# Performance work log

Measured on AMD Instinct MI355X. Metric: run time of the kernel, lower is better.

## Reference

```python
import jax, jax.numpy as jnp
import numpy as np

BITWIDTH = 7
M, K, N = 32768, 1024, 1024  # tokens, in_features, out_features


def _clip8(x):
    return jnp.clip(x, -127, 127).astype(jnp.int8)


def _range_bits(x):
    # RangeEstimate: ceil(log2(max|x|)) as int, 0 if all-zero
    r = jnp.max(jnp.abs(x).astype(jnp.float32))
    bits = jnp.ceil(jnp.log2(jnp.maximum(r, 1.0)))
    return jnp.where(r == 0, 0, bits).astype(jnp.int32)


def _round_shift(x, shift):
    # RoundShift (stochastic-style bit-shift rounding); shift is a traced int32 >= 1
    p = jnp.left_shift(jnp.int32(1), shift)
    rt = jnp.floor_divide(x, p)
    prob = x - rt * p
    dec = jnp.floor_divide(prob, jnp.left_shift(jnp.int32(1), shift - 1))
    return _clip8(rt + dec)


def setup_inputs() -> dict:
    key = jax.random.key(0)
    k1, k2 = jax.random.split(key)
    act_in = jax.random.randint(k1, (M, K), -127, 128, dtype=jnp.int32).astype(jnp.int8)
    weight = jax.random.randint(k2, (N, K), -127, 128, dtype=jnp.int32).astype(jnp.int8)
    exp_in = jnp.int32(0)
    weight_exp = jnp.int32(-11)  # ceil(log2(xavier bound)) - 7 for 1024x1024
    return {"act_in": act_in, "weight": weight, "exp_in": exp_in, "weight_exp": weight_exp}


def reference(act_in, weight, exp_in, weight_exp):
    # int8 GEMM with int32 accumulation: [M,K] @ [K,N]
    acc = jnp.matmul(act_in.astype(jnp.int32), weight.T.astype(jnp.int32))
    # act_calc: range-estimate + conditional bit-shift requantize to int8
    bits = _range_bits(acc)
    shift = bits - BITWIDTH
    pos = shift > 0
    sc = jnp.maximum(shift, 1)  # safe shift for the untaken branch
    act_out = jnp.where(pos, _round_shift(acc, sc), acc.astype(jnp.int8))
    exp_out = jnp.where(pos, exp_in + weight_exp + shift, exp_in + weight_exp)
    return act_out, exp_out
```

## Files before the change

### kernel.cpp

```cpp
#include <hip/hip_runtime.h>
#include <stdint.h>


#define MM 32768
#define NN 1024
#define KK 1024
#define BM 256
#define BN 256
#define BK 64
#define NKT (KK / BK)

typedef __attribute__((ext_vector_type(4))) int i32x4;
typedef __attribute__((ext_vector_type(16))) int i32x16;

__device__ __forceinline__ int pack4(int a, int b, int c, int d) {
  return (int)((unsigned)(a & 0xff) | ((unsigned)(b & 0xff) << 8) |
               ((unsigned)(c & 0xff) << 16) | ((unsigned)(d & 0xff) << 24));
}

__global__ void k_init(unsigned* slot) {
  if (threadIdx.x == 0) *slot = 0u;
}

__global__ void k_pack(const int* __restrict__ src, int8_t* __restrict__ dst, int n) {
  long t = (long)blockIdx.x * blockDim.x + threadIdx.x;
  long stride = (long)gridDim.x * blockDim.x;
  for (long i = t * 16; i < (long)n; i += stride * 16) {
    const i32x4* s = (const i32x4*)(src + i);
    i32x4 a0 = s[0], a1 = s[1], a2 = s[2], a3 = s[3];
    i32x4 o;
    o[0] = pack4(a0[0], a0[1], a0[2], a0[3]);
    o[1] = pack4(a1[0], a1[1], a1[2], a1[3]);
    o[2] = pack4(a2[0], a2[1], a2[2], a2[3]);
    o[3] = pack4(a3[0], a3[1], a3[2], a3[3]);
    *(i32x4*)(dst + i) = o;
  }
}

__global__ __launch_bounds__(512, 2)
void k_gemm(const int8_t* __restrict__ A8, const int8_t* __restrict__ B8,
            int* __restrict__ out, unsigned* __restrict__ maxslot) {
  __shared__ int8_t As[2][BM * BK];
  __shared__ int8_t Bs[2][BN * BK];

  const int tid  = threadIdx.x;
  const int lane = tid & 63;
  const int w    = tid >> 6;
  const int wm   = w >> 2;
  const int wn   = w & 3;

  const int orig = blockIdx.x;
  const int wgid = ((orig & 7) << 6) + (orig >> 3);
  const int bn = wgid & 3;
  const int bm = wgid >> 2;
  const int m0 = bm * BM;
  const int n0 = bn * BN;

  i32x16 acc[4][2];
#pragma unroll
  for (int i = 0; i < 4; ++i)
#pragma unroll
    for (int j = 0; j < 2; ++j) acc[i][j] = 0;

  auto stage = [&](int buf, int kt) {
    const int k0 = kt * BK;
#pragma unroll
    for (int q = 0; q < 2; ++q) {
      const int p   = (w * 2 + q) * 1024 + lane * 16;
      const int row = p >> 6;
      const int col = (p & 63) ^ (((row >> 1) & 3) << 4);
      __builtin_amdgcn_global_load_lds(
          (const __attribute__((address_space(1))) void*)(A8 + (size_t)(m0 + row) * KK + k0 + col),
          (__attribute__((address_space(3))) void*)(&As[buf][(w * 2 + q) * 1024]),
          16, 0, 0);
      __builtin_amdgcn_global_load_lds(
          (const __attribute__((address_space(1))) void*)(B8 + (size_t)(n0 + row) * KK + k0 + col),
          (__attribute__((address_space(3))) void*)(&Bs[buf][(w * 2 + q) * 1024]),
          16, 0, 0);
    }
  };

  auto compute = [&](int buf) {
#pragma unroll
    for (int ks = 0; ks < 2; ++ks) {
      i32x4 af[4], bf[2];
#pragma unroll
      for (int ni = 0; ni < 2; ++ni) {
        const int row = wn * 64 + ni * 32 + (lane & 31);
        const int a = row * BK +
            ((ks * 32 + ((lane >> 5) << 4)) ^ (((row >> 1) & 3) << 4));
        bf[ni] = *(const i32x4*)(&Bs[buf][a]);
      }
#pragma unroll
      for (int mi = 0; mi < 4; ++mi) {
        const int row = wm * 128 + mi * 32 + (lane & 31);
        const int a = row * BK +
            ((ks * 32 + ((lane >> 5) << 4)) ^ (((row >> 1) & 3) << 4));
        af[mi] = *(const i32x4*)(&As[buf][a]);
      }
      __builtin_amdgcn_s_setprio(1);
#pragma unroll
      for (int mi = 0; mi < 4; ++mi)
#pragma unroll
        for (int ni = 0; ni < 2; ++ni)
          acc[mi][ni] = __builtin_amdgcn_mfma_i32_32x32x32_i8(
              af[mi], bf[ni], acc[mi][ni], 0, 0, 0);
      __builtin_amdgcn_s_setprio(0);
    }
  };

  stage(0, 0);
  __syncthreads();
  for (int kt = 0; kt < NKT; ++kt) {
    if (kt + 1 < NKT) stage((kt + 1) & 1, kt + 1);
    compute(kt & 1);
    __syncthreads();
  }

  int mx = 0;
#pragma unroll
  for (int mi = 0; mi < 4; ++mi)
#pragma unroll
    for (int ni = 0; ni < 2; ++ni)
#pragma unroll
      for (int rg = 0; rg < 16; ++rg) {
        int x = acc[mi][ni][rg];
        int a = x < 0 ? -x : x;
        mx = a > mx ? a : mx;
      }
#pragma unroll
  for (int off = 32; off >= 1; off >>= 1) {
    int o = __shfl_xor(mx, off);
    mx = o > mx ? o : mx;
  }
  if (lane == 0) atomicMax(maxslot, (unsigned)mx);

#pragma unroll
  for (int mi = 0; mi < 4; ++mi)
#pragma unroll
    for (int ni = 0; ni < 2; ++ni) {
      const int mbase = m0 + wm * 128 + mi * 32;
      const int ncol  = n0 + wn * 64 + ni * 32 + (lane & 31);
#pragma unroll
      for (int rg = 0; rg < 16; ++rg) {
        const int mrow = mbase + (rg & 3) + ((rg >> 2) << 3) + ((lane >> 5) << 2);
        out[(size_t)mrow * NN + ncol] = acc[mi][ni][rg];
      }
    }
}

__global__ __launch_bounds__(256, 2)
void k_gemm_fb(const int* __restrict__ A32, const int* __restrict__ B32,
               int* __restrict__ out, unsigned* __restrict__ maxslot) {
  __shared__ int8_t As[128 * 128];
  __shared__ int8_t Bs[128 * 128];
  const int tid = threadIdx.x, lane = tid & 63, w = tid >> 6;
  const int wr = w >> 1, wc = w & 1;
  const int bn = blockIdx.x & 7, bm = blockIdx.x >> 3;
  const int m0 = bm * 128, n0 = bn * 128;
  i32x16 acc[2][2];
#pragma unroll
  for (int i = 0; i < 2; ++i)
#pragma unroll
    for (int j = 0; j < 2; ++j) acc[i][j] = 0;
  for (int kt = 0; kt < 8; ++kt) {
    const int k0 = kt * 128;
    __syncthreads();
#pragma unroll
    for (int j = 0; j < 4; ++j) {
      const int fb = (j * 256 + tid) * 16;
      const int row = fb >> 7;
      const int swz = fb ^ ((row & 7) << 4);
      const int col = fb & 127;
      const int* sa = A32 + (size_t)(m0 + row) * KK + k0 + col;
      const int* sb = B32 + (size_t)(n0 + row) * KK + k0 + col;
      i32x4 av, bv;
#pragma unroll
      for (int t = 0; t < 4; ++t) {
        i32x4 ta = ((const i32x4*)sa)[t];
        i32x4 tb = ((const i32x4*)sb)[t];
        av[t] = pack4(ta[0], ta[1], ta[2], ta[3]);
        bv[t] = pack4(tb[0], tb[1], tb[2], tb[3]);
      }
      *(i32x4*)(As + swz) = av;
      *(i32x4*)(Bs + swz) = bv;
    }
    __syncthreads();
#pragma unroll
    for (int ks = 0; ks < 4; ++ks) {
      i32x4 af[2], bf[2];
#pragma unroll
      for (int mi = 0; mi < 2; ++mi) {
        const int row = wr * 64 + mi * 32 + (lane & 31);
        int a = row * 128 + ks * 32 + ((lane >> 5) << 4);
        a ^= (row & 7) << 4;
        af[mi] = *(const i32x4*)(As + a);
      }
#pragma unroll
      for (int ni = 0; ni < 2; ++ni) {
        const int row = wc * 64 + ni * 32 + (lane & 31);
        int a = row * 128 + ks * 32 + ((lane >> 5) << 4);
        a ^= (row & 7) << 4;
        bf[ni] = *(const i32x4*)(Bs + a);
      }
#pragma unroll
      for (int mi = 0; mi < 2; ++mi)
#pragma unroll
        for (int ni = 0; ni < 2; ++ni)
          acc[mi][ni] = __builtin_amdgcn_mfma_i32_32x32x32_i8(
              af[mi], bf[ni], acc[mi][ni], 0, 0, 0);
    }
  }
  int mx = 0;
#pragma unroll
  for (int mi = 0; mi < 2; ++mi)
#pragma unroll
    for (int ni = 0; ni < 2; ++ni)
#pragma unroll
      for (int rg = 0; rg < 16; ++rg) {
        int x = acc[mi][ni][rg];
        int a = x < 0 ? -x : x;
        mx = a > mx ? a : mx;
      }
#pragma unroll
  for (int off = 32; off >= 1; off >>= 1) {
    int o = __shfl_xor(mx, off);
    mx = o > mx ? o : mx;
  }
  if (lane == 0) atomicMax(maxslot, (unsigned)mx);
#pragma unroll
  for (int mi = 0; mi < 2; ++mi)
#pragma unroll
    for (int ni = 0; ni < 2; ++ni) {
      const int mbase = m0 + wr * 64 + mi * 32;
      const int ncol = n0 + wc * 64 + ni * 32 + (lane & 31);
#pragma unroll
      for (int rg = 0; rg < 16; ++rg) {
        const int mrow = mbase + (rg & 3) + ((rg >> 2) << 3) + ((lane >> 5) << 2);
        out[(size_t)mrow * NN + ncol] = acc[mi][ni][rg];
      }
    }
}

__global__ __launch_bounds__(256)
void k_requant(int* __restrict__ out, const unsigned* __restrict__ maxslot) {
  const unsigned r = *maxslot;
  const int bits  = (r <= 1u) ? 0 : (32 - __clz((int)(r - 1u)));
  const int shift = bits - 7;
  const size_t n = (size_t)MM * NN;
  size_t i = ((size_t)blockIdx.x * blockDim.x + threadIdx.x) * 4;
  const size_t stride = (size_t)gridDim.x * blockDim.x * 4;
  if (shift > 0) {
    for (; i < n; i += stride) {
      i32x4 v = *(i32x4*)(out + i);
#pragma unroll
      for (int j = 0; j < 4; ++j) {
        const int x = v[j];
        int t = (x >> shift) + ((x >> (shift - 1)) & 1);
        v[j] = t > 127 ? 127 : (t < -127 ? -127 : t);
      }
      *(i32x4*)(out + i) = v;
    }
  } else {
    for (; i < n; i += stride) {
      i32x4 v = *(i32x4*)(out + i);
#pragma unroll
      for (int j = 0; j < 4; ++j) v[j] = (int)(int8_t)v[j];
      *(i32x4*)(out + i) = v;
    }
  }
}

__global__ void k_final(int* __restrict__ out, const int* __restrict__ exp_in,
                        const int* __restrict__ wexp) {
  if (threadIdx.x == 0) {
    const unsigned r = *(const unsigned*)(out + (size_t)MM * NN);
    const int bits  = (r <= 1u) ? 0 : (32 - __clz((int)(r - 1u)));
    const int shift = bits - 7;
    out[(size_t)MM * NN] = *exp_in + *wexp + (shift > 0 ? shift : 0);
  }
}

extern "C" void kernel_launch(void* const* d_in, const int* in_sizes, int n_in,
                              void* d_out, int out_size, void* d_ws, size_t ws_size,
                              hipStream_t stream) {
  const int* act    = (const int*)d_in[0];
  const int* wgt    = (const int*)d_in[1];
  const int* exp_in = (const int*)d_in[2];
  const int* wexp   = (const int*)d_in[3];
  int* out          = (int*)d_out;
  unsigned* maxslot = (unsigned*)(out + (size_t)MM * NN);

  const size_t need = (size_t)(MM + NN) * KK + 256;

  k_init<<<1, 64, 0, stream>>>(maxslot);

  if (ws_size >= need) {
    int8_t* a8 = (int8_t*)d_ws;
    int8_t* w8 = a8 + (size_t)MM * KK;
    k_pack<<<2048, 256, 0, stream>>>(act, a8, MM * KK);
    k_pack<<<256, 256, 0, stream>>>(wgt, w8, NN * KK);
    const int grid = (MM / BM) * (NN / BN);
    k_gemm<<<grid, 512, 0, stream>>>(a8, w8, out, maxslot);
  } else {
    k_gemm_fb<<<(MM / 128) * (NN / 128), 256, 0, stream>>>(act, wgt, out, maxslot);
  }

  k_requant<<<4096, 256, 0, stream>>>(out, maxslot);
  k_final<<<1, 64, 0, stream>>>(out, exp_in, wexp);
}
```

Baseline: 173.8 us.

## Shrink GEMM tile to 256x128 and use triple-buffered LDS with partial waitcnt

Halves the N tile so each of the 8 warps computes a 64x64 sub-tile, which doubles the block count and cuts accumulator registers per thread. The LDS double buffer becomes a triple buffer with prefetch two k-steps ahead. __syncthreads is replaced by an explicit s_waitcnt vmcnt(3) plus s_barrier, so loads for the next stage can stay in flight during compute. Smaller tiles raise global traffic per MFMA, and the hand-counted vmcnt has to match the number of loads issued per stage (3 per stage here).

After: 195.9 us. +12.7%, slower.

```diff
diff --git a/kernel.cpp b/kernel.cpp
--- a/kernel.cpp
+++ b/kernel.cpp
@@ -6,12 +6,16 @@
 #define NN 1024
 #define KK 1024
 #define BM 256
-#define BN 256
+#define BN 128
 #define BK 64
 #define NKT (KK / BK)
+#define TSA (BM * BK)
+#define TSB (BN * BK)
 
 typedef __attribute__((ext_vector_type(4))) int i32x4;
 typedef __attribute__((ext_vector_type(16))) int i32x16;
+
+#define BARRIER() asm volatile("s_barrier" ::: "memory")
 
 __device__ __forceinline__ int pack4(int a, int b, int c, int d) {
   return (int)((unsigned)(a & 0xff) | ((unsigned)(b & 0xff) << 8) |
@@ -40,25 +44,25 @@
 __global__ __launch_bounds__(512, 2)
 void k_gemm(const int8_t* __restrict__ A8, const int8_t* __restrict__ B8,
             int* __restrict__ out, unsigned* __restrict__ maxslot) {
-  __shared__ int8_t As[2][BM * BK];
-  __shared__ int8_t Bs[2][BN * BK];
+  __shared__ int8_t As[3][TSA];
+  __shared__ int8_t Bs[3][TSB];
 
   const int tid  = threadIdx.x;
   const int lane = tid & 63;
   const int w    = tid >> 6;
-  const int wm   = w >> 2;
-  const int wn   = w & 3;
+  const int wm   = w >> 1;
+  const int wn   = w & 1;
 
   const int orig = blockIdx.x;
-  const int wgid = ((orig & 7) << 6) + (orig >> 3);
-  const int bn = wgid & 3;
-  const int bm = wgid >> 2;
+  const int wgid = ((orig & 7) << 7) + (orig >> 3);
+  const int bn = wgid & 7;
+  const int bm = wgid >> 3;
   const int m0 = bm * BM;
   const int n0 = bn * BN;
 
-  i32x16 acc[4][2];
-#pragma unroll
-  for (int i = 0; i < 4; ++i)
+  i32x16 acc[2][2];
+#pragma unroll
+  for (int i = 0; i < 2; ++i)
 #pragma unroll
     for (int j = 0; j < 2; ++j) acc[i][j] = 0;
 
@@ -73,9 +77,14 @@
           (const __attribute__((address_space(1))) void*)(A8 + (size_t)(m0 + row) * KK + k0 + col),
           (__attribute__((address_space(3))) void*)(&As[buf][(w * 2 + q) * 1024]),
           16, 0, 0);
+    }
+    {
+      const int p   = w * 1024 + lane * 16;
+      const int row = p >> 6;
+      const int col = (p & 63) ^ (((row >> 1) & 3) << 4);
       __builtin_amdgcn_global_load_lds(
           (const __attribute__((address_space(1))) void*)(B8 + (size_t)(n0 + row) * KK + k0 + col),
-          (__attribute__((address_space(3))) void*)(&Bs[buf][(w * 2 + q) * 1024]),
+          (__attribute__((address_space(3))) void*)(&Bs[buf][w * 1024]),
           16, 0, 0);
     }
   };
@@ -83,7 +92,7 @@
   auto compute = [&](int buf) {
 #pragma unroll
     for (int ks = 0; ks < 2; ++ks) {
-      i32x4 af[4], bf[2];
+      i32x4 af[2], bf[2];
 #pragma unroll
       for (int ni = 0; ni < 2; ++ni) {
         const int row = wn * 64 + ni * 32 + (lane & 31);
@@ -92,15 +101,15 @@
         bf[ni] = *(const i32x4*)(&Bs[buf][a]);
       }
 #pragma unroll
-      for (int mi = 0; mi < 4; ++mi) {
-        const int row = wm * 128 + mi * 32 + (lane & 31);
+      for (int mi = 0; mi < 2; ++mi) {
+        const int row = wm * 64 + mi * 32 + (lane & 31);
         const int a = row * BK +
             ((ks * 32 + ((lane >> 5) << 4)) ^ (((row >> 1) & 3) << 4));
         af[mi] = *(const i32x4*)(&As[buf][a]);
       }
       __builtin_amdgcn_s_setprio(1);
 #pragma unroll
-      for (int mi = 0; mi < 4; ++mi)
+      for (int mi = 0; mi < 2; ++mi)
 #pragma unroll
         for (int ni = 0; ni < 2; ++ni)
           acc[mi][ni] = __builtin_amdgcn_mfma_i32_32x32x32_i8(
@@ -110,16 +119,26 @@
   };
 
   stage(0, 0);
-  __syncthreads();
+  stage(1, 1);
+  asm volatile("s_waitcnt vmcnt(3)" ::: "memory");
+  BARRIER();
+
+  int b0 = 0, b1 = 1, b2 = 2;
   for (int kt = 0; kt < NKT; ++kt) {
-    if (kt + 1 < NKT) stage((kt + 1) & 1, kt + 1);
-    compute(kt & 1);
-    __syncthreads();
+    const bool more2 = (kt + 2 < NKT);
+    if (more2) stage(b2, kt + 2);
+    compute(b0);
+    if (kt + 1 < NKT) {
+      if (more2) { asm volatile("s_waitcnt vmcnt(3)" ::: "memory"); }
+      else       { asm volatile("s_waitcnt vmcnt(0)" ::: "memory"); }
+      BARRIER();
+    }
+    const int t = b0; b0 = b1; b1 = b2; b2 = t;
   }
 
   int mx = 0;
 #pragma unroll
-  for (int mi = 0; mi < 4; ++mi)
+  for (int mi = 0; mi < 2; ++mi)
 #pragma unroll
     for (int ni = 0; ni < 2; ++ni)
 #pragma unroll
@@ -136,10 +155,10 @@
   if (lane == 0) atomicMax(maxslot, (unsigned)mx);
 
 #pragma unroll
-  for (int mi = 0; mi < 4; ++mi)
+  for (int mi = 0; mi < 2; ++mi)
 #pragma unroll
     for (int ni = 0; ni < 2; ++ni) {
-      const int mbase = m0 + wm * 128 + mi * 32;
+      const int mbase = m0 + wm * 64 + mi * 32;
       const int ncol  = n0 + wn * 64 + ni * 32 + (lane & 31);
 #pragma unroll
       for (int rg = 0; rg < 16; ++rg) {
```

## Fuse int32-to-int8 activation packing into GEMM tile loads and merge small kernels

Applied to the files above, without the earlier changes.

Removes the separate activation pack pass. The GEMM now loads int32 activations directly, packs them to int8 in registers and stores them into the swizzled LDS tile. The max-slot reset moves into the weight pack kernel, and the exponent output is written by the requant kernel, which cuts two tiny launches. The trade-off is that A is now loaded synchronously at four times the bytes, reread by each N-block, instead of through async global-to-LDS loads. That could hurt GEMM pipelining. In the fallback path the exponent write can also race with other blocks reading maxslot.

Measured after the change: 176.8 us. No clear change (+1.7%).

```diff
diff --git a/kernel.cpp b/kernel.cpp
--- a/kernel.cpp
+++ b/kernel.cpp
@@ -18,11 +18,9 @@
                ((unsigned)(c & 0xff) << 16) | ((unsigned)(d & 0xff) << 24));
 }
 
-__global__ void k_init(unsigned* slot) {
-  if (threadIdx.x == 0) *slot = 0u;
-}
-
-__global__ void k_pack(const int* __restrict__ src, int8_t* __restrict__ dst, int n) {
+__global__ void k_packw(const int* __restrict__ src, int8_t* __restrict__ dst,
+                        unsigned* __restrict__ maxslot, int n) {
+  if (blockIdx.x == 0 && threadIdx.x == 0) *maxslot = 0u;
   long t = (long)blockIdx.x * blockDim.x + threadIdx.x;
   long stride = (long)gridDim.x * blockDim.x;
   for (long i = t * 16; i < (long)n; i += stride * 16) {
@@ -38,7 +36,7 @@
 }
 
 __global__ __launch_bounds__(512, 2)
-void k_gemm(const int8_t* __restrict__ A8, const int8_t* __restrict__ B8,
+void k_gemm(const int* __restrict__ A32, const int8_t* __restrict__ B8,
             int* __restrict__ out, unsigned* __restrict__ maxslot) {
   __shared__ int8_t As[2][BM * BK];
   __shared__ int8_t Bs[2][BN * BK];
@@ -70,13 +68,17 @@
       const int row = p >> 6;
       const int col = (p & 63) ^ (((row >> 1) & 3) << 4);
       __builtin_amdgcn_global_load_lds(
-          (const __attribute__((address_space(1))) void*)(A8 + (size_t)(m0 + row) * KK + k0 + col),
-          (__attribute__((address_space(3))) void*)(&As[buf][(w * 2 + q) * 1024]),
-          16, 0, 0);
-      __builtin_amdgcn_global_load_lds(
           (const __attribute__((address_space(1))) void*)(B8 + (size_t)(n0 + row) * KK + k0 + col),
           (__attribute__((address_space(3))) void*)(&Bs[buf][(w * 2 + q) * 1024]),
           16, 0, 0);
+      const int* sa = A32 + (size_t)(m0 + row) * KK + k0 + col;
+      i32x4 av;
+#pragma unroll
+      for (int t = 0; t < 4; ++t) {
+        i32x4 ta = ((const i32x4*)sa)[t];
+        av[t] = pack4(ta[0], ta[1], ta[2], ta[3]);
+      }
+      *(i32x4*)(&As[buf][p]) = av;
     }
   };
 
@@ -147,6 +149,42 @@
         out[(size_t)mrow * NN + ncol] = acc[mi][ni][rg];
       }
     }
+}
+
+__global__ __launch_bounds__(256)
+void k_requant(int* __restrict__ out, const unsigned* __restrict__ maxslot,
+               const int* __restrict__ exp_in, const int* __restrict__ wexp) {
+  const unsigned r = *maxslot;
+  const int bits  = (r <= 1u) ? 0 : (32 - __clz((int)(r - 1u)));
+  const int shift = bits - 7;
+  if (blockIdx.x == 0 && threadIdx.x == 0)
+    out[(size_t)MM * NN] = *exp_in + *wexp + (shift > 0 ? shift : 0);
+  const size_t n = (size_t)MM * NN;
+  size_t i = ((size_t)blockIdx.x * blockDim.x + threadIdx.x) * 4;
+  const size_t stride = (size_t)gridDim.x * blockDim.x * 4;
+  if (shift > 0) {
+    for (; i < n; i += stride) {
+      i32x4 v = *(i32x4*)(out + i);
+#pragma unroll
+      for (int j = 0; j < 4; ++j) {
+        const int x = v[j];
+        int t = (x >> shift) + ((x >> (shift - 1)) & 1);
+        v[j] = t > 127 ? 127 : (t < -127 ? -127 : t);
+      }
+      *(i32x4*)(out + i) = v;
+    }
+  } else {
+    for (; i < n; i += stride) {
+      i32x4 v = *(i32x4*)(out + i);
+#pragma unroll
+      for (int j = 0; j < 4; ++j) v[j] = (int)(int8_t)v[j];
+      *(i32x4*)(out + i) = v;
+    }
+  }
+}
+
+__global__ void k_init(unsigned* slot) {
+  if (threadIdx.x == 0) *slot = 0u;
 }
 
 __global__ __launch_bounds__(256, 2)
@@ -242,45 +280,6 @@
     }
 }
 
-__global__ __launch_bounds__(256)
-void k_requant(int* __restrict__ out, const unsigned* __restrict__ maxslot) {
-  const unsigned r = *maxslot;
-  const int bits  = (r <= 1u) ? 0 : (32 - __clz((int)(r - 1u)));
-  const int shift = bits - 7;
-  const size_t n = (size_t)MM * NN;
-  size_t i = ((size_t)blockIdx.x * blockDim.x + threadIdx.x) * 4;
-  const size_t stride = (size_t)gridDim.x * blockDim.x * 4;
-  if (shift > 0) {
-    for (; i < n; i += stride) {
-      i32x4 v = *(i32x4*)(out + i);
-#pragma unroll
-      for (int j = 0; j < 4; ++j) {
-        const int x = v[j];
-        int t = (x >> shift) + ((x >> (shift - 1)) & 1);
-        v[j] = t > 127 ? 127 : (t < -127 ? -127 : t);
-      }
-      *(i32x4*)(out + i) = v;
-    }
-  } else {
-    for (; i < n; i += stride) {
-      i32x4 v = *(i32x4*)(out + i);
-#pragma unroll
-      for (int j = 0; j < 4; ++j) v[j] = (int)(int8_t)v[j];
-      *(i32x4*)(out + i) = v;
-    }
-  }
-}
-
-__global__ void k_final(int* __restrict__ out, const int* __restrict__ exp_in,
-                        const int* __restrict__ wexp) {
-  if (threadIdx.x == 0) {
-    const unsigned r = *(const unsigned*)(out + (size_t)MM * NN);
-    const int bits  = (r <= 1u) ? 0 : (32 - __clz((int)(r - 1u)));
-    const int shift = bits - 7;
-    out[(size_t)MM * NN] = *exp_in + *wexp + (shift > 0 ? shift : 0);
-  }
-}
-
 extern "C" void kernel_launch(void* const* d_in, const int* in_sizes, int n_in,
                               void* d_out, int out_size, void* d_ws, size_t ws_size,
                               hipStream_t stream) {
@@ -289,23 +288,19 @@
   const int* exp_in = (const int*)d_in[2];
   const int* wexp   = (const int*)d_in[3];
   int* out          = (int*)d_out;
-  unsigned* maxslot = (unsigned*)(out + (size_t)MM * NN);
-
-  const size_t need = (size_t)(MM + NN) * KK + 256;
-
-  k_init<<<1, 64, 0, stream>>>(maxslot);
+
+  const size_t need = (size_t)NN * KK + 256;
 
   if (ws_size >= need) {
-    int8_t* a8 = (int8_t*)d_ws;
-    int8_t* w8 = a8 + (size_t)MM * KK;
-    k_pack<<<2048, 256, 0, stream>>>(act, a8, MM * KK);
-    k_pack<<<256, 256, 0, stream>>>(wgt, w8, NN * KK);
-    const int grid = (MM / BM) * (NN / BN);
-    k_gemm<<<grid, 512, 0, stream>>>(a8, w8, out, maxslot);
+    int8_t* w8 = (int8_t*)d_ws;
+    unsigned* maxslot = (unsigned*)(w8 + (size_t)NN * KK);
+    k_packw<<<256, 256, 0, stream>>>(wgt, w8, maxslot, NN * KK);
+    k_gemm<<<(MM / BM) * (NN / BN), 512, 0, stream>>>(act, w8, out, maxslot);
+    k_requant<<<4096, 256, 0, stream>>>(out, maxslot, exp_in, wexp);
   } else {
+    unsigned* maxslot = (unsigned*)(out + (size_t)MM * NN);
+    k_init<<<1, 64, 0, stream>>>(maxslot);
     k_gemm_fb<<<(MM / 128) * (NN / 128), 256, 0, stream>>>(act, wgt, out, maxslot);
-  }
-
-  k_requant<<<4096, 256, 0, stream>>>(out, maxslot);
-  k_final<<<1, 64, 0, stream>>>(out, exp_in, wexp);
-}
+    k_requant<<<4096, 256, 0, stream>>>(out, maxslot, exp_in, wexp);
+  }
+}
```
